# Kernel tuning notes

Measured on AMD Instinct MI355X. Metric: run time of the kernel, lower is better.

Reference implementation:

```python
import jax, jax.numpy as jnp
import numpy as np

B, T, D = 64, 512, 1024  # batch, step_dim, feature_dim


def setup_inputs() -> dict:
    key = jax.random.key(0)
    k1, k2, k3, k4, k5 = jax.random.split(key, 5)
    x = jax.random.normal(k1, (B, T, D), dtype=jnp.float32)
    mask = jax.random.randint(k2, (B, T), 0, 2).astype(bool)
    mask = mask.at[:, 0].set(True)  # guarantee >=1 valid token per row
    # xavier_uniform bounds
    w_bound = float(np.sqrt(6.0 / (D + D)))
    c_bound = float(np.sqrt(6.0 / (T + 1)))
    weight = jax.random.uniform(k3, (D, D), minval=-w_bound, maxval=w_bound, dtype=jnp.float32)
    context_vector = jax.random.uniform(k4, (T, 1), minval=-c_bound, maxval=c_bound, dtype=jnp.float32)
    b = jnp.zeros((T,), dtype=jnp.float32)
    return {"x": x, "mask": mask, "weight": weight, "context_vector": context_vector, "b": b}


def reference(x, mask, weight, context_vector, b):
    # batched bilinear scores: eij[b,t,s] = x[b,t,:] @ W @ x[b,s,:]^T
    xw = jnp.einsum('btd,de->bte', x, weight)          # [B,T,D]
    eij = jnp.einsum('bte,bse->bts', xw, x)            # [B,T,T]
    # bias over last axis (matches view(-1, T) + b), tanh
    eij = jnp.tanh(eij + b)                            # [B,T,T]
    # context-vector reduction over last axis -> [B,T]
    scores = jnp.einsum('bts,s->bt', eij, context_vector[:, 0])
    # masked softmax over T
    scores = jnp.where(mask, scores, -jnp.inf)
    a = jax.nn.softmax(scores, axis=1)                 # [B,T]
    # weighted sum of inputs -> [B,D]
    out = jnp.einsum('btd,bt->bd', x, a)
    return (out, a)
```

## Files before the change

kernel.cpp:

```cpp
#include <hip/hip_runtime.h>
#include <hip/hip_bf16.h>
#include <math.h>

#define B_ 64
#define T_ 512
#define D_ 1024
#define M_ (B_*T_)

typedef unsigned short u16;
typedef __attribute__((ext_vector_type(8))) _Float16 f16x8;
typedef __attribute__((ext_vector_type(4))) float f32x4;

__device__ __forceinline__ u16 f2h(float f) {
  union { _Float16 h; u16 u; } v;
  v.h = (_Float16)f;
  return v.u;
}

__device__ __forceinline__ float h2f(u16 u) {
  union { u16 u; _Float16 h; } v;
  v.u = u;
  return (float)v.h;
}

__device__ __forceinline__ float fast_tanh(float x) {
  return 1.0f - 2.0f / (__expf(2.0f * x) + 1.0f);
}

__device__ __forceinline__ void gll16(const void* g, void* l) {
  __builtin_amdgcn_global_load_lds(
      (const __attribute__((address_space(1))) unsigned int*)g,
      (__attribute__((address_space(3))) unsigned int*)l, 16, 0, 0);
}

__global__ __launch_bounds__(256) void cvt_kernel(const float4* __restrict__ x,
                                                  ushort4* __restrict__ xh,
                                                  const float* __restrict__ W,
                                                  u16* __restrict__ wt) {
  __shared__ float tile[32][33];
  const int bid = blockIdx.x;
  if (bid < 32768) {
    int i = bid * 256 + threadIdx.x;
    float4 v = x[i];
    ushort4 o;
    o.x = f2h(v.x); o.y = f2h(v.y); o.z = f2h(v.z); o.w = f2h(v.w);
    xh[i] = o;
  } else {
    const int tb = bid - 32768;
    const int n0 = (tb & 31) * 32, k0 = (tb >> 5) * 32;
    const int tx = threadIdx.x & 31, ty = threadIdx.x >> 5;
#pragma unroll
    for (int ph = 0; ph < 4; ph++)
      tile[ty + ph * 8][tx] = W[(k0 + ty + ph * 8) * D_ + n0 + tx];
    __syncthreads();
#pragma unroll
    for (int ph = 0; ph < 4; ph++)
      wt[(long)(n0 + ty + ph * 8) * D_ + k0 + tx] = f2h(tile[tx][ty + ph * 8]);
  }
}

__global__ __launch_bounds__(256, 2) void gemm1_kernel(const u16* __restrict__ xh,
                                                       const u16* __restrict__ wt,
                                                       u16* __restrict__ xw) {
  __shared__ u16 As[256 * 64];
  __shared__ u16 Bs[128 * 64];
  f32x4 acc[8][4] = {};
  const int tid = threadIdx.x;
  const int bx = blockIdx.x;
  const int xcd = bx & 7, j = bx >> 3;
  const int mt = xcd * 16 + (j >> 3);
  const int nt = j & 7;
  const long m0 = (long)mt * 256;
  const long n0 = (long)nt * 128;
  const u16* Abase = xh + m0 * D_;
  const u16* Bbase = wt + n0 * D_;

  const int wave = tid >> 6, lane = tid & 63;
  const int p = lane & 7, rl = lane >> 3;

  const u16* gA[8]; u16* lA[8];
#pragma unroll
  for (int i = 0; i < 8; i++) {
    int g = wave * 8 + i;
    int r = g * 8 + rl;
    int c = (p - (r >> 1)) & 7;
    gA[i] = Abase + (long)r * D_ + c * 8;
    lA[i] = As + g * 512;
  }
  const u16* gB[4]; u16* lB[4];
#pragma unroll
  for (int i = 0; i < 4; i++) {
    int g = wave * 4 + i;
    int r = g * 8 + rl;
    int c = (p - (r >> 1)) & 7;
    gB[i] = Bbase + (long)r * D_ + c * 8;
    lB[i] = Bs + g * 512;
  }

  const int wrow = (wave >> 1) * 128, wcol = (wave & 1) * 64;
  const int lm = lane & 15, qd = lane >> 4;
  const u16* ra = As + (wrow + lm) * 64;
  const u16* rb = Bs + (wcol + lm) * 64;
  const int pk0 = ((qd + (lm >> 1)) & 7) * 8;
  const int pk1 = ((qd + 4 + (lm >> 1)) & 7) * 8;

  for (int kt = 0; kt < D_; kt += 64) {
#pragma unroll
    for (int i = 0; i < 8; i++) { gll16(gA[i], lA[i]); gA[i] += 64; }
#pragma unroll
    for (int i = 0; i < 4; i++) { gll16(gB[i], lB[i]); gB[i] += 64; }
    __syncthreads();
#pragma unroll
    for (int kk = 0; kk < 2; kk++) {
      const int pk = kk ? pk1 : pk0;
      f16x8 af[8], bfr[4];
#pragma unroll
      for (int i = 0; i < 8; i++) af[i] = *(const f16x8*)(ra + i * 16 * 64 + pk);
#pragma unroll
      for (int i = 0; i < 4; i++) bfr[i] = *(const f16x8*)(rb + i * 16 * 64 + pk);
#pragma unroll
      for (int mi = 0; mi < 8; mi++)
#pragma unroll
        for (int ni = 0; ni < 4; ni++)
          acc[mi][ni] = __builtin_amdgcn_mfma_f32_16x16x32_f16(af[mi], bfr[ni], acc[mi][ni], 0, 0, 0);
    }
    __syncthreads();
  }

  const int lm2 = lane & 15, qd2 = lane >> 4;
#pragma unroll
  for (int mi = 0; mi < 8; mi++)
#pragma unroll
    for (int ni = 0; ni < 4; ni++) {
      long m = m0 + wrow + mi * 16 + qd2 * 4;
      long n = n0 + wcol + ni * 16 + lm2;
      u16* ptr = xw + m * D_ + n;
#pragma unroll
      for (int r = 0; r < 4; r++) ptr[(long)r * D_] = f2h(acc[mi][ni][r]);
    }
}

__device__ __forceinline__ void gemm_core128(const u16* __restrict__ Abase,
                                             const u16* __restrict__ Bbase, int K,
                                             u16* As, u16* Bs, int tid, f32x4 acc[4][4]) {
  const int wave = tid >> 6, lane = tid & 63;
  const int swz_c = ((lane & 3) - ((lane >> 3) & 3)) & 3;
  const int rin = lane >> 2;
  const u16* gA[2]; u16* lA[2];
  const u16* gB[2]; u16* lB[2];
#pragma unroll
  for (int j = 0; j < 2; j++) {
    int ci = wave * 2 + j;
    gA[j] = Abase + (long)(ci * 16 + rin) * K + swz_c * 8;
    lA[j] = As + ci * 512;
    gB[j] = Bbase + (long)(ci * 16 + rin) * K + swz_c * 8;
    lB[j] = Bs + ci * 512;
  }
  const int wrow = (wave >> 1) * 64, wcol = (wave & 1) * 64;
  const int lm = lane & 15, qd = lane >> 4;
  const int swz_r = ((qd + (lm >> 1)) & 3) * 8;
  const u16* ra = As + (wrow + lm) * 32 + swz_r;
  const u16* rb = Bs + (wcol + lm) * 32 + swz_r;

  for (int kt = 0; kt < K; kt += 32) {
#pragma unroll
    for (int j = 0; j < 2; j++) {
      gll16(gA[j], lA[j]); gA[j] += 32;
      gll16(gB[j], lB[j]); gB[j] += 32;
    }
    __syncthreads();
    f16x8 af[4], bfr[4];
#pragma unroll
    for (int i = 0; i < 4; i++) {
      af[i] = *(const f16x8*)(ra + i * 512);
      bfr[i] = *(const f16x8*)(rb + i * 512);
    }
#pragma unroll
    for (int mi = 0; mi < 4; mi++)
#pragma unroll
      for (int ni = 0; ni < 4; ni++)
        acc[mi][ni] = __builtin_amdgcn_mfma_f32_16x16x32_f16(af[mi], bfr[ni], acc[mi][ni], 0, 0, 0);
    __syncthreads();
  }
}

__global__ __launch_bounds__(256, 4) void gemm2_kernel(const u16* __restrict__ xw,
                                                       const u16* __restrict__ xh,
                                                       const float* __restrict__ bias,
                                                       const float* __restrict__ cv,
                                                       float* __restrict__ scores_part) {
  __shared__ u16 As[128 * 32], Bs[128 * 32];
  f32x4 acc[4][4] = {};
  const int bx = blockIdx.x;
  const int xcd = bx & 7, j = bx >> 3;
  const int bb = xcd * 8 + (j >> 4);
  const int tile = j & 15;
  const int tt = tile >> 2, st = tile & 3;
  const int tid = threadIdx.x;
  const long arow = (long)bb * T_ + tt * 128;
  const long brow = (long)bb * T_ + st * 128;
  gemm_core128(xw + arow * D_, xh + brow * D_, D_, As, Bs, tid, acc);

  const int wave = tid >> 6, lane = tid & 63;
  const int wrow = (wave >> 1) * 64, wcol = (wave & 1) * 64;
  const int lm = lane & 15, qd = lane >> 4;
  float cvv[4], bv[4];
#pragma unroll
  for (int ni = 0; ni < 4; ni++) {
    int s = st * 128 + wcol + ni * 16 + lm;
    cvv[ni] = cv[s];
    bv[ni] = bias[s];
  }
  const int plane = st * 2 + (wave & 1);
  float* dst = scores_part + plane * (B_ * T_) + bb * T_ + tt * 128;
#pragma unroll
  for (int mi = 0; mi < 4; mi++) {
#pragma unroll
    for (int r = 0; r < 4; r++) {
      float p = 0.f;
#pragma unroll
      for (int ni = 0; ni < 4; ni++) p += fast_tanh(acc[mi][ni][r] + bv[ni]) * cvv[ni];
      p += __shfl_xor(p, 1); p += __shfl_xor(p, 2);
      p += __shfl_xor(p, 4); p += __shfl_xor(p, 8);
      if (lm == 0) dst[wrow + mi * 16 + qd * 4 + r] = p;
    }
  }
}

__global__ __launch_bounds__(256) void sm_wsum_kernel(const float* __restrict__ sp,
                                                      const unsigned char* __restrict__ m8,
                                                      const u16* __restrict__ xh,
                                                      float* __restrict__ a_out,
                                                      float* __restrict__ out) {
  __shared__ float a_sh[512];
  __shared__ float red[8];
  __shared__ int nonz;
  __shared__ float4 lred[4][64];
  const int b = blockIdx.x, dq = blockIdx.y, tid = threadIdx.x;
  const int w = tid >> 6, ln = tid & 63;
  if (tid == 0) nonz = 0;
  __syncthreads();
  {
    unsigned char c = m8[tid * 4 + 1] | m8[tid * 4 + 2] | m8[tid * 4 + 3] |
                      m8[(tid + 256) * 4 + 1] | m8[(tid + 256) * 4 + 2] | m8[(tid + 256) * 4 + 3];
    if (c) atomicOr(&nonz, 1);
  }
  __syncthreads();
  const bool is_i32 = (nonz == 0);
  float v[2]; bool valid[2];
#pragma unroll
  for (int h = 0; h < 2; h++) {
    int t = tid + h * 256;
    int idx = b * T_ + t;
    valid[h] = is_i32 ? (m8[(long)idx * 4] != 0) : (m8[idx] != 0);
    float s = 0.f;
#pragma unroll
    for (int pl = 0; pl < 8; pl++) s += sp[pl * (B_ * T_) + idx];
    v[h] = valid[h] ? s : -INFINITY;
  }
  float m = fmaxf(v[0], v[1]);
#pragma unroll
  for (int o = 32; o > 0; o >>= 1) m = fmaxf(m, __shfl_xor(m, o));
  if (ln == 0) red[w] = m;
  __syncthreads();
  const float rowmax = fmaxf(fmaxf(red[0], red[1]), fmaxf(red[2], red[3]));
  float e0 = valid[0] ? expf(v[0] - rowmax) : 0.f;
  float e1 = valid[1] ? expf(v[1] - rowmax) : 0.f;
  float ss = e0 + e1;
#pragma unroll
  for (int o = 32; o > 0; o >>= 1) ss += __shfl_xor(ss, o);
  if (ln == 0) red[4 + w] = ss;
  __syncthreads();
  const float tot = red[4] + red[5] + red[6] + red[7];
  const float a0 = e0 / tot, a1 = e1 / tot;
  a_sh[tid] = a0; a_sh[tid + 256] = a1;
  if (dq == 0) {
    a_out[b * T_ + tid] = a0;
    a_out[b * T_ + tid + 256] = a1;
  }
  __syncthreads();
  const int d0 = dq * 256 + ln * 4;
  const u16* xp = xh + (long)b * T_ * D_ + d0;
  float4 acc = make_float4(0.f, 0.f, 0.f, 0.f);
  for (int i = 0; i < 128; i++) {
    int t = w * 128 + i;
    float av = a_sh[t];
    ushort4 xv = *(const ushort4*)(xp + (long)t * D_);
    acc.x += av * h2f(xv.x); acc.y += av * h2f(xv.y);
    acc.z += av * h2f(xv.z); acc.w += av * h2f(xv.w);
  }
  lred[w][ln] = acc;
  __syncthreads();
  if (w == 0) {
    float4 s0 = lred[0][ln], s1 = lred[1][ln], s2 = lred[2][ln], s3 = lred[3][ln];
    float4 s;
    s.x = s0.x + s1.x + s2.x + s3.x;
    s.y = s0.y + s1.y + s2.y + s3.y;
    s.z = s0.z + s1.z + s2.z + s3.z;
    s.w = s0.w + s1.w + s2.w + s3.w;
    *(float4*)(out + (long)b * D_ + d0) = s;
  }
}

extern "C" void kernel_launch(void* const* d_in, const int* in_sizes, int n_in,
                              void* d_out, int out_size, void* d_ws, size_t ws_size,
                              hipStream_t stream) {
  const float* x = (const float*)d_in[0];
  const unsigned char* mask = (const unsigned char*)d_in[1];
  const float* W = (const float*)d_in[2];
  const float* cv = (const float*)d_in[3];
  const float* bias = (const float*)d_in[4];

  float* out = (float*)d_out;
  float* a_out = out + (size_t)B_ * D_;

  char* ws = (char*)d_ws;
  u16* xh = (u16*)(ws);
  u16* wt = (u16*)(ws + 67108864);
  float* scores_part = (float*)(ws + 67108864);
  u16* xw = (u16*)(ws + 69206016);

  cvt_kernel<<<32768 + 1024, 256, 0, stream>>>((const float4*)x, (ushort4*)xh, W, wt);
  gemm1_kernel<<<1024, 256, 0, stream>>>(xh, wt, xw);
  gemm2_kernel<<<1024, 256, 0, stream>>>(xw, xh, bias, cv, scores_part);
  sm_wsum_kernel<<<dim3(B_, 4), 256, 0, stream>>>(scores_part, mask, xh, a_out, out);
}
```

Baseline: 322.5 us.

## Share a 256x256 four-stage pipelined MFMA GEMM core across both GEMMs

```diff
diff --git a/kernel.cpp b/kernel.cpp
--- a/kernel.cpp
+++ b/kernel.cpp
@@ -59,162 +59,139 @@
   }
 }
 
-__global__ __launch_bounds__(256, 2) void gemm1_kernel(const u16* __restrict__ xh,
+struct Stage {
+  const u16* gA[2]; const u16* gB[2];
+  u16* lA[2]; u16* lB[2];
+  int t;
+  __device__ __forceinline__ void issue() {
+    const int sb = (t & 3) * 8192;
+#pragma unroll
+    for (int j = 0; j < 2; j++) {
+      gll16(gA[j], lA[j] + sb);
+      gll16(gB[j], lB[j] + sb);
+      gA[j] += 32; gB[j] += 32;
+    }
+    t++;
+  }
+};
+
+template<int VMN>
+__device__ __forceinline__ void core_step(Stage& st, bool do_issue,
+                                          const u16* ra, const u16* rb, int buf,
+                                          f32x4 (&acc)[8][4]) {
+  if constexpr (VMN == 8)      asm volatile("s_waitcnt vmcnt(8)" ::: "memory");
+  else if constexpr (VMN == 4) asm volatile("s_waitcnt vmcnt(4)" ::: "memory");
+  else                         asm volatile("s_waitcnt vmcnt(0)" ::: "memory");
+  __builtin_amdgcn_s_barrier();
+  asm volatile("" ::: "memory");
+  __builtin_amdgcn_sched_barrier(0);
+  if (do_issue) st.issue();
+  const u16* rat = ra + buf * 8192;
+  const u16* rbt = rb + buf * 8192;
+  f16x8 af[8], bfr[4];
+#pragma unroll
+  for (int i = 0; i < 8; i++) af[i] = *(const f16x8*)(rat + i * 512);
+#pragma unroll
+  for (int i = 0; i < 4; i++) bfr[i] = *(const f16x8*)(rbt + i * 512);
+  __builtin_amdgcn_s_setprio(1);
+#pragma unroll
+  for (int mi = 0; mi < 8; mi++)
+#pragma unroll
+    for (int ni = 0; ni < 4; ni++)
+      acc[mi][ni] = __builtin_amdgcn_mfma_f32_16x16x32_f16(af[mi], bfr[ni], acc[mi][ni], 0, 0, 0);
+  __builtin_amdgcn_s_setprio(0);
+}
+
+__device__ __forceinline__ void gemm_core256(const u16* __restrict__ Abase,
+                                             const u16* __restrict__ Bbase,
+                                             u16* As, u16* Bs, int tid,
+                                             f32x4 (&acc)[8][4]) {
+  const int wave = tid >> 6, lane = tid & 63;
+  const int swz_c = ((lane & 3) - ((lane >> 3) & 3)) & 3;
+  const int rin = lane >> 2;
+  Stage st; st.t = 0;
+#pragma unroll
+  for (int j = 0; j < 2; j++) {
+    const int ci = wave * 2 + j;
+    st.gA[j] = Abase + (long)(ci * 16 + rin) * D_ + swz_c * 8;
+    st.lA[j] = As + ci * 512;
+    st.gB[j] = Bbase + (long)(ci * 16 + rin) * D_ + swz_c * 8;
+    st.lB[j] = Bs + ci * 512;
+  }
+  st.issue(); st.issue(); st.issue();
+  const int wrow = (wave >> 2) * 128, wcol = (wave & 3) * 64;
+  const int lm = lane & 15, qd = lane >> 4;
+  const int swz_r = ((qd + (lm >> 1)) & 3) * 8;
+  const u16* ra = As + (wrow + lm) * 32 + swz_r;
+  const u16* rb = Bs + (wcol + lm) * 32 + swz_r;
+#pragma unroll 1
+  for (int t = 0; t < 30; t++)
+    core_step<8>(st, t < 29, ra, rb, t & 3, acc);
+  core_step<4>(st, false, ra, rb, 30 & 3, acc);
+  core_step<0>(st, false, ra, rb, 31 & 3, acc);
+}
+
+__global__ __launch_bounds__(512, 2) void gemm1_kernel(const u16* __restrict__ xh,
                                                        const u16* __restrict__ wt,
                                                        u16* __restrict__ xw) {
-  __shared__ u16 As[256 * 64];
-  __shared__ u16 Bs[128 * 64];
+  __shared__ u16 As[4 * 8192];
+  __shared__ u16 Bs[4 * 8192];
   f32x4 acc[8][4] = {};
   const int tid = threadIdx.x;
   const int bx = blockIdx.x;
   const int xcd = bx & 7, j = bx >> 3;
-  const int mt = xcd * 16 + (j >> 3);
-  const int nt = j & 7;
-  const long m0 = (long)mt * 256;
-  const long n0 = (long)nt * 128;
-  const u16* Abase = xh + m0 * D_;
-  const u16* Bbase = wt + n0 * D_;
+  const int mt = xcd * 16 + (j >> 2);
+  const int nt = j & 3;
+  const long m0 = (long)mt * 256, n0 = (long)nt * 256;
+  gemm_core256(xh + m0 * D_, wt + n0 * D_, As, Bs, tid, acc);
 
   const int wave = tid >> 6, lane = tid & 63;
-  const int p = lane & 7, rl = lane >> 3;
-
-  const u16* gA[8]; u16* lA[8];
-#pragma unroll
-  for (int i = 0; i < 8; i++) {
-    int g = wave * 8 + i;
-    int r = g * 8 + rl;
-    int c = (p - (r >> 1)) & 7;
-    gA[i] = Abase + (long)r * D_ + c * 8;
-    lA[i] = As + g * 512;
-  }
-  const u16* gB[4]; u16* lB[4];
-#pragma unroll
-  for (int i = 0; i < 4; i++) {
-    int g = wave * 4 + i;
-    int r = g * 8 + rl;
-    int c = (p - (r >> 1)) & 7;
-    gB[i] = Bbase + (long)r * D_ + c * 8;
-    lB[i] = Bs + g * 512;
-  }
-
-  const int wrow = (wave >> 1) * 128, wcol = (wave & 1) * 64;
+  const int wrow = (wave >> 2) * 128, wcol = (wave & 3) * 64;
   const int lm = lane & 15, qd = lane >> 4;
-  const u16* ra = As + (wrow + lm) * 64;
-  const u16* rb = Bs + (wcol + lm) * 64;
-  const int pk0 = ((qd + (lm >> 1)) & 7) * 8;
-  const int pk1 = ((qd + 4 + (lm >> 1)) & 7) * 8;
-
-  for (int kt = 0; kt < D_; kt += 64) {
-#pragma unroll
-    for (int i = 0; i < 8; i++) { gll16(gA[i], lA[i]); gA[i] += 64; }
-#pragma unroll
-    for (int i = 0; i < 4; i++) { gll16(gB[i], lB[i]); gB[i] += 64; }
-    __syncthreads();
-#pragma unroll
-    for (int kk = 0; kk < 2; kk++) {
-      const int pk = kk ? pk1 : pk0;
-      f16x8 af[8], bfr[4];
-#pragma unroll
-      for (int i = 0; i < 8; i++) af[i] = *(const f16x8*)(ra + i * 16 * 64 + pk);
-#pragma unroll
-      for (int i = 0; i < 4; i++) bfr[i] = *(const f16x8*)(rb + i * 16 * 64 + pk);
-#pragma unroll
-      for (int mi = 0; mi < 8; mi++)
-#pragma unroll
-        for (int ni = 0; ni < 4; ni++)
-          acc[mi][ni] = __builtin_amdgcn_mfma_f32_16x16x32_f16(af[mi], bfr[ni], acc[mi][ni], 0, 0, 0);
-    }
-    __syncthreads();
-  }
-
-  const int lm2 = lane & 15, qd2 = lane >> 4;
 #pragma unroll
   for (int mi = 0; mi < 8; mi++)
 #pragma unroll
     for (int ni = 0; ni < 4; ni++) {
-      long m = m0 + wrow + mi * 16 + qd2 * 4;
-      long n = n0 + wcol + ni * 16 + lm2;
+      long m = m0 + wrow + mi * 16 + qd * 4;
+      long n = n0 + wcol + ni * 16 + lm;
       u16* ptr = xw + m * D_ + n;
 #pragma unroll
       for (int r = 0; r < 4; r++) ptr[(long)r * D_] = f2h(acc[mi][ni][r]);
     }
 }
 
-__device__ __forceinline__ void gemm_core128(const u16* __restrict__ Abase,
-                                             const u16* __restrict__ Bbase, int K,
-                                             u16* As, u16* Bs, int tid, f32x4 acc[4][4]) {
-  const int wave = tid >> 6, lane = tid & 63;
-  const int swz_c = ((lane & 3) - ((lane >> 3) & 3)) & 3;
-  const int rin = lane >> 2;
-  const u16* gA[2]; u16* lA[2];
-  const u16* gB[2]; u16* lB[2];
-#pragma unroll
-  for (int j = 0; j < 2; j++) {
-    int ci = wave * 2 + j;
-    gA[j] = Abase + (long)(ci * 16 + rin) * K + swz_c * 8;
-    lA[j] = As + ci * 512;
-    gB[j] = Bbase + (long)(ci * 16 + rin) * K + swz_c * 8;
-    lB[j] = Bs + ci * 512;
-  }
-  const int wrow = (wave >> 1) * 64, wcol = (wave & 1) * 64;
-  const int lm = lane & 15, qd = lane >> 4;
-  const int swz_r = ((qd + (lm >> 1)) & 3) * 8;
-  const u16* ra = As + (wrow + lm) * 32 + swz_r;
-  const u16* rb = Bs + (wcol + lm) * 32 + swz_r;
-
-  for (int kt = 0; kt < K; kt += 32) {
-#pragma unroll
-    for (int j = 0; j < 2; j++) {
-      gll16(gA[j], lA[j]); gA[j] += 32;
-      gll16(gB[j], lB[j]); gB[j] += 32;
-    }
-    __syncthreads();
-    f16x8 af[4], bfr[4];
-#pragma unroll
-    for (int i = 0; i < 4; i++) {
-      af[i] = *(const f16x8*)(ra + i * 512);
-      bfr[i] = *(const f16x8*)(rb + i * 512);
-    }
-#pragma unroll
-    for (int mi = 0; mi < 4; mi++)
-#pragma unroll
-      for (int ni = 0; ni < 4; ni++)
-        acc[mi][ni] = __builtin_amdgcn_mfma_f32_16x16x32_f16(af[mi], bfr[ni], acc[mi][ni], 0, 0, 0);
-    __syncthreads();
-  }
-}
-
-__global__ __launch_bounds__(256, 4) void gemm2_kernel(const u16* __restrict__ xw,
+__global__ __launch_bounds__(512, 2) void gemm2_kernel(const u16* __restrict__ xw,
                                                        const u16* __restrict__ xh,
                                                        const float* __restrict__ bias,
                                                        const float* __restrict__ cv,
                                                        float* __restrict__ scores_part) {
-  __shared__ u16 As[128 * 32], Bs[128 * 32];
-  f32x4 acc[4][4] = {};
+  __shared__ u16 As[4 * 8192];
+  __shared__ u16 Bs[4 * 8192];
+  f32x4 acc[8][4] = {};
+  const int tid = threadIdx.x;
   const int bx = blockIdx.x;
   const int xcd = bx & 7, j = bx >> 3;
-  const int bb = xcd * 8 + (j >> 4);
-  const int tile = j & 15;
-  const int tt = tile >> 2, st = tile & 3;
-  const int tid = threadIdx.x;
-  const long arow = (long)bb * T_ + tt * 128;
-  const long brow = (long)bb * T_ + st * 128;
-  gemm_core128(xw + arow * D_, xh + brow * D_, D_, As, Bs, tid, acc);
+  const int bb = xcd * 8 + (j >> 2);
+  const int tile = j & 3;
+  const int tt = tile >> 1, st_ = tile & 1;
+  const long arow = (long)bb * T_ + tt * 256;
+  const long brow = (long)bb * T_ + st_ * 256;
+  gemm_core256(xw + arow * D_, xh + brow * D_, As, Bs, tid, acc);
 
   const int wave = tid >> 6, lane = tid & 63;
-  const int wrow = (wave >> 1) * 64, wcol = (wave & 1) * 64;
+  const int wrow = (wave >> 2) * 128, wcol = (wave & 3) * 64;
   const int lm = lane & 15, qd = lane >> 4;
   float cvv[4], bv[4];
 #pragma unroll
   for (int ni = 0; ni < 4; ni++) {
-    int s = st * 128 + wcol + ni * 16 + lm;
+    int s = st_ * 256 + wcol + ni * 16 + lm;
     cvv[ni] = cv[s];
     bv[ni] = bias[s];
   }
-  const int plane = st * 2 + (wave & 1);
-  float* dst = scores_part + plane * (B_ * T_) + bb * T_ + tt * 128;
-#pragma unroll
-  for (int mi = 0; mi < 4; mi++) {
+  const int plane = st_ * 4 + (wave & 3);
+  float* dst = scores_part + plane * (B_ * T_) + bb * T_ + tt * 256;
+#pragma unroll
+  for (int mi = 0; mi < 8; mi++) {
 #pragma unroll
     for (int r = 0; r < 4; r++) {
       float p = 0.f;
@@ -321,7 +298,7 @@
   u16* xw = (u16*)(ws + 69206016);
 
   cvt_kernel<<<32768 + 1024, 256, 0, stream>>>((const float4*)x, (ushort4*)xh, W, wt);
-  gemm1_kernel<<<1024, 256, 0, stream>>>(xh, wt, xw);
-  gemm2_kernel<<<1024, 256, 0, stream>>>(xw, xh, bias, cv, scores_part);
+  gemm1_kernel<<<512, 512, 0, stream>>>(xh, wt, xw);
+  gemm2_kernel<<<256, 512, 0, stream>>>(xw, xh, bias, cv, scores_part);
   sm_wsum_kernel<<<dim3(B_, 4), 256, 0, stream>>>(scores_part, mask, xh, a_out, out);
 }
```

Measured after the change: 342.2 us. +6.1%, slower.
